# Kernel tuning notes

Measured on AMD Instinct MI355X. Metric: run time of the kernel, lower is better.

The kernel has to match this reference:

```python
import jax, jax.numpy as jnp
import numpy as np

B, C, F, H, W = 4, 256, 16, 32, 32


def setup_inputs() -> dict:
    key = jax.random.key(0)
    ks = jax.random.split(key, 8)
    x = jax.random.normal(ks[0], (B, C, F, H, W), dtype=jnp.float32)
    wq = jax.random.normal(ks[1], (C, C), dtype=jnp.float32) * 0.05
    bq = jax.random.normal(ks[2], (C,), dtype=jnp.float32) * 0.05
    wk = jax.random.normal(ks[3], (C, C), dtype=jnp.float32) * 0.05
    bk = jax.random.normal(ks[4], (C,), dtype=jnp.float32) * 0.05
    wv = jax.random.normal(ks[5], (C, C), dtype=jnp.float32) * 0.05
    bv = jax.random.normal(ks[6], (C,), dtype=jnp.float32) * 0.05
    gamma = jax.random.normal(ks[7], (1,), dtype=jnp.float32) * 0.1
    return {"x": x, "wq": wq, "bq": bq, "wk": wk, "bk": bk, "wv": wv, "bv": bv, "gamma": gamma}


def reference(x, wq, bq, wk, bk, wv, bv, gamma):
    b, c, f, h, w = x.shape
    p = h * w
    # replicate torch .view(batch*frames, channels, H, W): raw memory reinterpretation
    xr = x.reshape(b * f, c, p)  # [B*F, C, HW]
    proj = lambda wt, bi: jnp.einsum('ncp,dc->ndp', xr, wt) + bi[None, :, None]
    q = proj(wq, bq).reshape(b, f, c, p).transpose(0, 2, 1, 3)  # [B, C, F, HW]
    k = proj(wk, bk).reshape(b, f, c, p).transpose(0, 2, 3, 1)  # [B, C, HW, F]
    v = proj(wv, bv).reshape(b, f, c, p).transpose(0, 2, 1, 3)  # [B, C, F, HW]
    attn = jax.nn.softmax(jnp.matmul(q, k) * (1.0 / c ** 0.5), axis=-1)  # [B, C, F, F]
    out = jnp.matmul(attn, v)  # [B, C, F, HW]
    # replicate permute(0,2,1,3).view(B,F,C,H,W).permute(0,2,1,3,4)
    out = out.transpose(0, 2, 1, 3).reshape(b, f, c, h, w).transpose(0, 2, 1, 3, 4)
    return gamma * out + x
```

## Files before the change

### kernel.cpp

```cpp
#include <hip/hip_runtime.h>
#include <hip/hip_bf16.h>

#define CC 256
#define FF 16
#define PP 1024
#define BB 4
#define NN 64

typedef __bf16 bf16x8 __attribute__((ext_vector_type(8)));
typedef float  f32x4  __attribute__((ext_vector_type(4)));

__device__ __forceinline__ void async16(const __hip_bfloat16* g, char* l) {
    __builtin_amdgcn_global_load_lds(
        (const __attribute__((address_space(1))) unsigned int*)g,
        (__attribute__((address_space(3))) unsigned int*)l, 16, 0, 0);
}

__global__ __launch_bounds__(256) void xt_kernel(
    const float* __restrict__ x, __hip_bfloat16* __restrict__ Xt)
{
    __shared__ float T[64][65];
    const int n = blockIdx.z, c0 = blockIdx.y * 64, p0 = blockIdx.x * 64;
    const int t = threadIdx.x;
    const int pl = t & 63, r0 = t >> 6;
    const float* xp = x + ((size_t)n * CC + c0) * PP + p0;
    #pragma unroll
    for (int i = 0; i < 16; ++i) {
        const int cl = r0 + i * 4;
        T[cl][pl] = xp[(size_t)cl * PP + pl];
    }
    __syncthreads();
    __hip_bfloat16* op = Xt + ((size_t)n * PP + p0) * CC + c0;
    const int cl2 = (t & 31) * 2, q0 = t >> 5;
    #pragma unroll
    for (int j = 0; j < 8; ++j) {
        const int pr = q0 + j * 8;
        __hip_bfloat162 h;
        h.x = __float2bfloat16(T[cl2][pr]);
        h.y = __float2bfloat16(T[cl2 + 1][pr]);
        *(__hip_bfloat162*)(op + (size_t)pr * CC + cl2) = h;
    }
}

__global__ __launch_bounds__(256) void wconv_kernel(
    const float* __restrict__ wq, const float* __restrict__ wk,
    const float* __restrict__ wv, __hip_bfloat16* __restrict__ Wb)
{
    const int proj = blockIdx.y;
    const float* src = proj == 0 ? wq : (proj == 1 ? wk : wv);
    __hip_bfloat16* dst = Wb + (size_t)proj * CC * CC;
    const int idx = (blockIdx.x * 256 + threadIdx.x) * 4;
    const float4 v = *(const float4*)(src + idx);
    dst[idx + 0] = __float2bfloat16(v.x);
    dst[idx + 1] = __float2bfloat16(v.y);
    dst[idx + 2] = __float2bfloat16(v.z);
    dst[idx + 3] = __float2bfloat16(v.w);
}

__global__ __launch_bounds__(256) void qkv_mfma(
    const __hip_bfloat16* __restrict__ Wb, const __hip_bfloat16* __restrict__ Xt,
    const float* __restrict__ bq, const float* __restrict__ bk,
    const float* __restrict__ bv,
    __hip_bfloat16* __restrict__ Qw, __hip_bfloat16* __restrict__ Kw,
    float* __restrict__ Vout)
{
    __shared__ char lds[16384];

    const int p0 = blockIdx.x * 128, d0 = blockIdx.y * 128;
    const int z = blockIdx.z, proj = z % 3, n = z / 3;
    const int t = threadIdx.x, w = t >> 6, lane = t & 63;
    const int wd = (w >> 1) * 64, wp = (w & 1) * 64;
    const int q = lane >> 4, m16 = lane & 15;

    const int srow = t >> 2;
    const int gcol = (t & 3) ^ ((srow >> 1) & 3);
    const __hip_bfloat16* Abase = Wb + (size_t)proj * CC * CC
                                + (size_t)(d0 + srow) * CC + gcol * 8;
    const __hip_bfloat16* Bbase = Xt + (size_t)n * PP * CC
                                + (size_t)(p0 + srow) * CC + gcol * 8;
    char* ldsA0 = lds + t * 16;
    char* ldsA1 = lds + (t + 256) * 16;
    char* ldsB0 = lds + 8192 + t * 16;
    char* ldsB1 = lds + 8192 + (t + 256) * 16;

    const int cxor = q ^ ((m16 >> 1) & 3);
    const int aoff = (wd + m16) * 64 + cxor * 16;
    const int boff = 8192 + (wp + m16) * 64 + cxor * 16;

    f32x4 acc[4][4];
    #pragma unroll
    for (int i = 0; i < 4; ++i)
        #pragma unroll
        for (int j = 0; j < 4; ++j)
            acc[i][j] = (f32x4){0.f, 0.f, 0.f, 0.f};

    for (int c0 = 0; c0 < CC; c0 += 32) {
        async16(Abase + c0, ldsA0);
        async16(Abase + 64 * CC + c0, ldsA1);
        async16(Bbase + c0, ldsB0);
        async16(Bbase + 64 * CC + c0, ldsB1);
        __syncthreads();

        bf16x8 a[4], b[4];
        #pragma unroll
        for (int i = 0; i < 4; ++i)
            a[i] = *(const bf16x8*)(lds + aoff + i * 1024);
        #pragma unroll
        for (int j = 0; j < 4; ++j)
            b[j] = *(const bf16x8*)(lds + boff + j * 1024);
        #pragma unroll
        for (int i = 0; i < 4; ++i)
            #pragma unroll
            for (int j = 0; j < 4; ++j)
                acc[i][j] = __builtin_amdgcn_mfma_f32_16x16x32_bf16(a[i], b[j], acc[i][j], 0, 0, 0);
        __syncthreads();
    }

    if (proj < 2) {
        const float* bias = (proj == 0) ? bq : bk;
        __hip_bfloat16* dst = ((proj == 0) ? Qw : Kw) + (size_t)n * CC * PP;
        #pragma unroll
        for (int i = 0; i < 4; ++i)
            #pragma unroll
            for (int r = 0; r < 4; ++r) {
                const int d = d0 + wd + i * 16 + q * 4 + r;
                const float bb = bias[d];
                #pragma unroll
                for (int j = 0; j < 4; ++j) {
                    const int p = p0 + wp + j * 16 + m16;
                    dst[(size_t)d * PP + p] = __float2bfloat16(acc[i][j][r] + bb);
                }
            }
    } else {
        const int b = n >> 4, f = n & 15;
        #pragma unroll
        for (int i = 0; i < 4; ++i)
            #pragma unroll
            for (int r = 0; r < 4; ++r) {
                const int d = d0 + wd + i * 16 + q * 4 + r;
                const float bb = bv[d];
                #pragma unroll
                for (int j = 0; j < 4; ++j) {
                    const int p = p0 + wp + j * 16 + m16;
                    Vout[(((size_t)(b * CC + d)) * FF + f) * PP + p] = acc[i][j][r] + bb;
                }
            }
    }
}

__global__ __launch_bounds__(256) void attn_out(
    const __hip_bfloat16* __restrict__ Qw, const __hip_bfloat16* __restrict__ Kw,
    const float* __restrict__ x, const float* __restrict__ gamma,
    float* __restrict__ out)
{
    const int d = blockIdx.x, b = blockIdx.y;
    const int t = threadIdx.x, w = t >> 6, lane = t & 63;
    const int q = lane >> 4, m16 = lane & 15;
    __shared__ float Sp[4][16][17];
    __shared__ float As[16][17];

    {
        const size_t gbase = ((size_t)(b * 16 + m16) * CC + d) * PP + w * 256 + q * 8;
        f32x4 acc0 = {0.f, 0.f, 0.f, 0.f}, acc1 = {0.f, 0.f, 0.f, 0.f};
        #pragma unroll
        for (int pc = 0; pc < 256; pc += 64) {
            bf16x8 aq0 = *(const bf16x8*)(Qw + gbase + pc);
            bf16x8 bk0 = *(const bf16x8*)(Kw + gbase + pc);
            bf16x8 aq1 = *(const bf16x8*)(Qw + gbase + pc + 32);
            bf16x8 bk1 = *(const bf16x8*)(Kw + gbase + pc + 32);
            acc0 = __builtin_amdgcn_mfma_f32_16x16x32_bf16(aq0, bk0, acc0, 0, 0, 0);
            acc1 = __builtin_amdgcn_mfma_f32_16x16x32_bf16(aq1, bk1, acc1, 0, 0, 0);
        }
        #pragma unroll
        for (int r = 0; r < 4; ++r)
            Sp[w][q * 4 + r][m16] = acc0[r] + acc1[r];
    }
    __syncthreads();

    {
        const int f1 = t >> 4, f2 = t & 15;
        const float s = (Sp[0][f1][f2] + Sp[1][f1][f2] + Sp[2][f1][f2] + Sp[3][f1][f2]) * 0.0625f;
        float m = s;
        #pragma unroll
        for (int off = 1; off < 16; off <<= 1) m = fmaxf(m, __shfl_xor(m, off));
        const float e = __expf(s - m);
        float den = e;
        #pragma unroll
        for (int off = 1; off < 16; off <<= 1) den += __shfl_xor(den, off);
        As[f1][f2] = e / den;
    }
    __syncthreads();

    const float g = gamma[0];
    const size_t base = ((size_t)(b * CC + d) * FF) * PP;
    #pragma unroll
    for (int i = 0; i < 2; ++i) {
        const int p = i * 512 + t * 2;
        float2 vv[16];
        #pragma unroll
        for (int f2 = 0; f2 < 16; ++f2)
            vv[f2] = *(const float2*)(out + base + (size_t)f2 * PP + p);
        #pragma unroll
        for (int f1 = 0; f1 < 16; ++f1) {
            float a0 = 0.f, a1 = 0.f;
            #pragma unroll
            for (int f2 = 0; f2 < 16; ++f2) {
                const float av = As[f1][f2];
                a0 += av * vv[f2].x;
                a1 += av * vv[f2].y;
            }
            const float2 xv = *(const float2*)(x + base + (size_t)f1 * PP + p);
            float2 res;
            res.x = g * a0 + xv.x;
            res.y = g * a1 + xv.y;
            *(float2*)(out + base + (size_t)f1 * PP + p) = res;
        }
    }
}

extern "C" void kernel_launch(void* const* d_in, const int* in_sizes, int n_in,
                              void* d_out, int out_size, void* d_ws, size_t ws_size,
                              hipStream_t stream) {
    const float* x     = (const float*)d_in[0];
    const float* wq    = (const float*)d_in[1];
    const float* bq    = (const float*)d_in[2];
    const float* wk    = (const float*)d_in[3];
    const float* bk    = (const float*)d_in[4];
    const float* wv    = (const float*)d_in[5];
    const float* bv    = (const float*)d_in[6];
    const float* gamma = (const float*)d_in[7];
    float* out = (float*)d_out;

    __hip_bfloat16* Qw = (__hip_bfloat16*)d_ws;
    __hip_bfloat16* Kw = Qw + (size_t)NN * CC * PP;
    __hip_bfloat16* Xt = Kw + (size_t)NN * CC * PP;
    __hip_bfloat16* Wb = Xt + (size_t)NN * CC * PP;

    wconv_kernel<<<dim3(CC * CC / (256 * 4), 3), 256, 0, stream>>>(wq, wk, wv, Wb);
    xt_kernel<<<dim3(PP / 64, CC / 64, NN), 256, 0, stream>>>(x, Xt);
    qkv_mfma<<<dim3(PP / 128, CC / 128, NN * 3), 256, 0, stream>>>(
        Wb, Xt, bq, bk, bv, Qw, Kw, out);
    attn_out<<<dim3(CC, BB), 256, 0, stream>>>(Qw, Kw, x, gamma, out);
}
```

Before: 205.8 us.

## Widen GEMM K-step, stage epilogue through LDS for vector stores, vectorize attn_out

The QKV GEMM now loads a 64-wide K slice per barrier pair with an 8-way XOR swizzle, halving the number of sync iterations. The epilogue writes accumulators to a padded LDS scratch and then emits 16-byte coalesced global stores for Q/K (bf16) and V (fp32), replacing scattered scalar stores. The attn_out kernel processes 4 floats per thread in one pass instead of two float2 passes. LDS usage grows to 36 KB per block, which may reduce occupancy, and the larger vv register array raises register pressure.

```diff
diff --git a/kernel.cpp b/kernel.cpp
--- a/kernel.cpp
+++ b/kernel.cpp
@@ -64,7 +64,7 @@
     __hip_bfloat16* __restrict__ Qw, __hip_bfloat16* __restrict__ Kw,
     float* __restrict__ Vout)
 {
-    __shared__ char lds[16384];
+    __shared__ char lds[36864];
 
     const int p0 = blockIdx.x * 128, d0 = blockIdx.y * 128;
     const int z = blockIdx.z, proj = z % 3, n = z / 3;
@@ -72,20 +72,8 @@
     const int wd = (w >> 1) * 64, wp = (w & 1) * 64;
     const int q = lane >> 4, m16 = lane & 15;
 
-    const int srow = t >> 2;
-    const int gcol = (t & 3) ^ ((srow >> 1) & 3);
-    const __hip_bfloat16* Abase = Wb + (size_t)proj * CC * CC
-                                + (size_t)(d0 + srow) * CC + gcol * 8;
-    const __hip_bfloat16* Bbase = Xt + (size_t)n * PP * CC
-                                + (size_t)(p0 + srow) * CC + gcol * 8;
-    char* ldsA0 = lds + t * 16;
-    char* ldsA1 = lds + (t + 256) * 16;
-    char* ldsB0 = lds + 8192 + t * 16;
-    char* ldsB1 = lds + 8192 + (t + 256) * 16;
-
-    const int cxor = q ^ ((m16 >> 1) & 3);
-    const int aoff = (wd + m16) * 64 + cxor * 16;
-    const int boff = 8192 + (wp + m16) * 64 + cxor * 16;
+    const __hip_bfloat16* Abase = Wb + (size_t)proj * CC * CC + (size_t)d0 * CC;
+    const __hip_bfloat16* Bbase = Xt + (size_t)n * PP * CC + (size_t)p0 * CC;
 
     f32x4 acc[4][4];
     #pragma unroll
@@ -94,57 +82,91 @@
         for (int j = 0; j < 4; ++j)
             acc[i][j] = (f32x4){0.f, 0.f, 0.f, 0.f};
 
-    for (int c0 = 0; c0 < CC; c0 += 32) {
-        async16(Abase + c0, ldsA0);
-        async16(Abase + 64 * CC + c0, ldsA1);
-        async16(Bbase + c0, ldsB0);
-        async16(Bbase + 64 * CC + c0, ldsB1);
+    for (int c0 = 0; c0 < CC; c0 += 64) {
+        #pragma unroll
+        for (int k = 0; k < 4; ++k) {
+            const int s = t + 256 * k;
+            const int row = s >> 3;
+            const int gc = (s & 7) ^ (row & 7);
+            async16(Abase + (size_t)row * CC + c0 + gc * 8, lds + s * 16);
+            async16(Bbase + (size_t)row * CC + c0 + gc * 8, lds + 16384 + s * 16);
+        }
         __syncthreads();
-
-        bf16x8 a[4], b[4];
-        #pragma unroll
-        for (int i = 0; i < 4; ++i)
-            a[i] = *(const bf16x8*)(lds + aoff + i * 1024);
-        #pragma unroll
-        for (int j = 0; j < 4; ++j)
-            b[j] = *(const bf16x8*)(lds + boff + j * 1024);
-        #pragma unroll
-        for (int i = 0; i < 4; ++i)
-            #pragma unroll
-            for (int j = 0; j < 4; ++j)
-                acc[i][j] = __builtin_amdgcn_mfma_f32_16x16x32_bf16(a[i], b[j], acc[i][j], 0, 0, 0);
+        #pragma unroll
+        for (int kk = 0; kk < 2; ++kk) {
+            bf16x8 a[4], b[4];
+            #pragma unroll
+            for (int i = 0; i < 4; ++i) {
+                const int row = wd + i * 16 + m16;
+                const int col = (4 * kk + q) ^ (row & 7);
+                a[i] = *(const bf16x8*)(lds + row * 128 + col * 16);
+            }
+            #pragma unroll
+            for (int j = 0; j < 4; ++j) {
+                const int row = wp + j * 16 + m16;
+                const int col = (4 * kk + q) ^ (row & 7);
+                b[j] = *(const bf16x8*)(lds + 16384 + row * 128 + col * 16);
+            }
+            #pragma unroll
+            for (int i = 0; i < 4; ++i)
+                #pragma unroll
+                for (int j = 0; j < 4; ++j)
+                    acc[i][j] = __builtin_amdgcn_mfma_f32_16x16x32_bf16(a[i], b[j], acc[i][j], 0, 0, 0);
+        }
         __syncthreads();
     }
+
+    __syncthreads();
+    char* wb = lds + w * 9216;
+    const int dl2 = lane >> 3, pl2 = lane & 7;
 
     if (proj < 2) {
         const float* bias = (proj == 0) ? bq : bk;
-        __hip_bfloat16* dst = ((proj == 0) ? Qw : Kw) + (size_t)n * CC * PP;
         #pragma unroll
         for (int i = 0; i < 4; ++i)
             #pragma unroll
             for (int r = 0; r < 4; ++r) {
-                const int d = d0 + wd + i * 16 + q * 4 + r;
-                const float bb = bias[d];
+                const int d_l = i * 16 + q * 4 + r;
+                const float bb = bias[d0 + wd + d_l];
                 #pragma unroll
                 for (int j = 0; j < 4; ++j) {
-                    const int p = p0 + wp + j * 16 + m16;
-                    dst[(size_t)d * PP + p] = __float2bfloat16(acc[i][j][r] + bb);
+                    const int p_l = j * 16 + m16;
+                    *(__hip_bfloat16*)(wb + d_l * 144 + p_l * 2) =
+                        __float2bfloat16(acc[i][j][r] + bb);
                 }
             }
+        __hip_bfloat16* dst = ((proj == 0) ? Qw : Kw) + (size_t)n * CC * PP;
+        #pragma unroll
+        for (int k = 0; k < 8; ++k) {
+            const int d_l = k * 8 + dl2;
+            bf16x8 v = *(const bf16x8*)(wb + d_l * 144 + pl2 * 16);
+            *(bf16x8*)(dst + (size_t)(d0 + wd + d_l) * PP + p0 + wp + pl2 * 8) = v;
+        }
     } else {
         const int b = n >> 4, f = n & 15;
         #pragma unroll
-        for (int i = 0; i < 4; ++i)
-            #pragma unroll
-            for (int r = 0; r < 4; ++r) {
-                const int d = d0 + wd + i * 16 + q * 4 + r;
-                const float bb = bv[d];
+        for (int h = 0; h < 2; ++h) {
+            #pragma unroll
+            for (int i = 0; i < 4; ++i)
                 #pragma unroll
-                for (int j = 0; j < 4; ++j) {
-                    const int p = p0 + wp + j * 16 + m16;
-                    Vout[(((size_t)(b * CC + d)) * FF + f) * PP + p] = acc[i][j][r] + bb;
+                for (int r = 0; r < 4; ++r) {
+                    const int d_l = i * 16 + q * 4 + r;
+                    const float bb = bv[d0 + wd + d_l];
+                    #pragma unroll
+                    for (int jj = 0; jj < 2; ++jj) {
+                        const int j = 2 * h + jj;
+                        const int p_rel = jj * 16 + m16;
+                        *(float*)(wb + d_l * 144 + p_rel * 4) = acc[i][j][r] + bb;
+                    }
                 }
-            }
+            #pragma unroll
+            for (int k = 0; k < 8; ++k) {
+                const int d_l = k * 8 + dl2;
+                f32x4 v = *(const f32x4*)(wb + d_l * 144 + pl2 * 16);
+                const int p = p0 + wp + h * 32 + pl2 * 4;
+                *(f32x4*)(Vout + (((size_t)(b * CC + d0 + wd + d_l)) * FF + f) * PP + p) = v;
+            }
+        }
     }
 }
 
@@ -192,29 +214,22 @@
     __syncthreads();
 
     const float g = gamma[0];
-    const size_t base = ((size_t)(b * CC + d) * FF) * PP;
-    #pragma unroll
-    for (int i = 0; i < 2; ++i) {
-        const int p = i * 512 + t * 2;
-        float2 vv[16];
-        #pragma unroll
-        for (int f2 = 0; f2 < 16; ++f2)
-            vv[f2] = *(const float2*)(out + base + (size_t)f2 * PP + p);
-        #pragma unroll
-        for (int f1 = 0; f1 < 16; ++f1) {
-            float a0 = 0.f, a1 = 0.f;
-            #pragma unroll
-            for (int f2 = 0; f2 < 16; ++f2) {
-                const float av = As[f1][f2];
-                a0 += av * vv[f2].x;
-                a1 += av * vv[f2].y;
-            }
-            const float2 xv = *(const float2*)(x + base + (size_t)f1 * PP + p);
-            float2 res;
-            res.x = g * a0 + xv.x;
-            res.y = g * a1 + xv.y;
-            *(float2*)(out + base + (size_t)f1 * PP + p) = res;
-        }
+    const size_t base = ((size_t)(b * CC + d) * FF) * PP + t * 4;
+    f32x4 vv[16];
+    #pragma unroll
+    for (int f2 = 0; f2 < 16; ++f2)
+        vv[f2] = *(const f32x4*)(out + base + (size_t)f2 * PP);
+    #pragma unroll
+    for (int f1 = 0; f1 < 16; ++f1) {
+        f32x4 a = {0.f, 0.f, 0.f, 0.f};
+        #pragma unroll
+        for (int f2 = 0; f2 < 16; ++f2) {
+            const float av = As[f1][f2];
+            a += av * vv[f2];
+        }
+        const f32x4 xv = *(const f32x4*)(x + base + (size_t)f1 * PP);
+        const f32x4 res = g * a + xv;
+        *(f32x4*)(out + base + (size_t)f1 * PP) = res;
     }
 }
 
```

Result: faster. 199.8 us (-2.9%).
